# Optimization experiments

Measured on AMD Instinct MI355X. Metric: run time of the kernel, lower is better.

The kernel has to match this reference:

```python
import jax, jax.numpy as jnp
import numpy as np

N = 400000       # number of non-zero points
C_IN = 64
C_OUT = 64
K = 3            # kernel size per dim -> 27 offsets
S = 1024         # coordinate grid bound; packed key = ((x*S)+y)*S+z < 2^30 fits int32


def _pack(c):
    # linear packing: pack(a+b) == pack(a)+pack(b); injective for coords in [0, S-1]^3
    return (c[..., 0].astype(jnp.int32) * S + c[..., 1]) * S + c[..., 2]


def setup_inputs() -> dict:
    rng = np.random.default_rng(0)
    # unique coordinates in [1, S-2]^3 so coord+offset stays in [0, S-1]^3
    cand = rng.integers(1, S - 1, size=(2 * N, 3), dtype=np.int32)
    keys = (cand[:, 0].astype(np.int64) * S + cand[:, 1]) * S + cand[:, 2]
    _, uidx = np.unique(keys, return_index=True)
    coords = cand[np.sort(uidx)][:N]
    assert coords.shape[0] == N
    # kernel offsets: {-1,0,1}^3 in row-major (minuet layout order)
    r = np.arange(-(K // 2), K // 2 + 1)
    offsets = np.stack(np.meshgrid(r, r, r, indexing='ij'), axis=-1).reshape(-1, 3).astype(np.int32)
    key = jax.random.key(0)
    k1, k2 = jax.random.split(key)
    features = jax.random.normal(k1, (N, C_IN), dtype=jnp.float32)
    kernel = jax.random.normal(k2, (K ** 3, C_IN, C_OUT), dtype=jnp.float32) / np.float32(np.sqrt(C_IN * K ** 3))
    return {
        'features': features,
        'kernel': kernel,
        'coords': jnp.asarray(coords),
        'offsets': jnp.asarray(offsets),
    }


def reference(features, kernel, coords, offsets):
    # Sparse conv with stride=1: outputs live at the same (sorted) coordinates.
    # out_i = sum_k 1[p_j == q_i + delta_k] F_j @ W_k  (gather-GEMM-scatter)
    keys = _pack(coords)                      # [N]
    order = jnp.argsort(keys)                 # build sorted coordinate index
    skeys = keys[order]                       # [N] sorted keys
    sfeat = features[order]                   # [N, C_in]
    n = skeys.shape[0]
    okeys = _pack(offsets)                    # [K^3] packed offsets (linearity of _pack)

    def step(acc, xs):
        ok, Wk = xs                           # scalar key offset, [C_in, C_out]
        qk = skeys + ok                       # query keys = target coord + delta_k
        idx = jnp.clip(jnp.searchsorted(skeys, qk), 0, n - 1)
        valid = skeys[idx] == qk              # kernel-map mask for this offset
        g = jnp.where(valid[:, None], sfeat[idx], 0.0)   # gather
        return acc + g @ Wk, None             # GEMM + scatter(accumulate)

    out0 = jnp.zeros((n, kernel.shape[-1]), dtype=features.dtype)
    out, _ = jax.lax.scan(step, out0, (okeys, kernel))
    return out
```

## Files before the change

### kernel.cpp

```cpp
#include <hip/hip_runtime.h>

#define NBUCK  4096
#define SCAP   256
#define QCHUNK 256
#define WPAD   320
#define WCAP   (QCHUNK + 2 * WPAD + 16)
#define MCAP   96

typedef __bf16 bf16_t;
typedef bf16_t bf16x8 __attribute__((ext_vector_type(8)));
typedef float  f32x4  __attribute__((ext_vector_type(4)));
typedef unsigned long long u64;

__global__ void k_bin(const int* __restrict__ coords, const float* __restrict__ kern,
                      u64* __restrict__ slot, int* __restrict__ cnt,
                      bf16_t* __restrict__ wf, int N, int nb) {
    if (blockIdx.x >= nb) {
        int tid = (blockIdx.x - nb) * 256 + threadIdx.x;
        int f = tid >> 9, l = (tid >> 3) & 63, j = tid & 7;
        int nt = f >> 1, kt = f & 1;
        int k = kt * 32 + ((l >> 4) * 8) + j;
        int n = nt * 16 + (l & 15);
        wf[tid] = (bf16_t)kern[13 * 4096 + k * 64 + n];
        return;
    }
    __shared__ int sc[768];
    int base3 = blockIdx.x * 768;
    for (int t = threadIdx.x; t < 768; t += 256) {
        int idx = base3 + t;
        sc[t] = (idx < 3 * N) ? coords[idx] : 0;
    }
    __syncthreads();
    int i = blockIdx.x * 256 + threadIdx.x;
    if (i < N) {
        int key = (sc[3 * threadIdx.x] << 20) | (sc[3 * threadIdx.x + 1] << 10) | sc[3 * threadIdx.x + 2];
        int b = key >> 18;
        int pos = atomicAdd(&cnt[b], 1);
        if (pos < SCAP)
            slot[(size_t)b * SCAP + pos] = ((u64)(unsigned)key << 20) | (unsigned)i;
    }
}

__global__ void k_sortp(const int* __restrict__ cnt, const u64* __restrict__ slot,
                        int* __restrict__ skeys, int* __restrict__ sorder) {
    int t = threadIdx.x;
    int vals[16];
    int s = 0;
#pragma unroll
    for (int j = 0; j < 16; ++j) {
        int v = cnt[t * 16 + j];
        if (v > SCAP) v = SCAP;
        vals[j] = v; s += v;
    }
    int lane = t & 63, wv = t >> 6;
    int x = s;
#pragma unroll
    for (int d = 1; d < 64; d <<= 1) {
        int y = __shfl_up(x, d, 64);
        if (lane >= d) x += y;
    }
    __shared__ int wsum[4];
    if (lane == 63) wsum[wv] = x;
    __syncthreads();
    int add = 0;
    for (int u = 0; u < wv; ++u) add += wsum[u];
    int run = (x + add) - s;
    __shared__ int sbase[5];
    int b0 = blockIdx.x * 4;
#pragma unroll
    for (int j = 0; j < 16; ++j) {
        int bb = t * 16 + j;
        int d = bb - b0;
        if (d >= 0 && d <= 4) sbase[d] = run;
        run += vals[j];
    }
    if (t == 255 && b0 + 4 == NBUCK) sbase[4] = x + add;
    __syncthreads();

    __shared__ u64 sk[4][SCAP];
    int b = b0 + wv;
    int lo = sbase[wv];
    int size = sbase[wv + 1] - sbase[wv];
    for (int e = lane; e < size; e += 64) sk[wv][e] = slot[(size_t)b * SCAP + e];
    __syncthreads();
    for (int e = lane; e < size; e += 64) {
        u64 my = sk[wv][e];
        int r = 0;
        for (int j = 0; j < size; ++j) r += (sk[wv][j] < my);
        skeys[lo + r]  = (int)(my >> 20);
        sorder[lo + r] = (int)(my & 0xFFFFF);
    }
}

__device__ __forceinline__ int lower_bound_g(const int* __restrict__ a, int n, int q) {
    int lo = 0, hi = n;
    while (lo < hi) { int mid = (lo + hi) >> 1; if (a[mid] < q) lo = mid + 1; else hi = mid; }
    return lo;
}

__global__ __launch_bounds__(256) void k_conv(const int* __restrict__ skeys,
                                              const int* __restrict__ sorder,
                                              const float* __restrict__ feat,
                                              const bf16_t* __restrict__ wf,
                                              const float* __restrict__ kern,
                                              float* __restrict__ out, int N) {
    const int tid = threadIdx.x;
    const int lane = tid & 63, wv = tid >> 6;
    const int i0 = blockIdx.x * QCHUNK;
    const int iend = min(i0 + QCHUNK, N);

    __shared__ int sw[WCAP];
    __shared__ int mlist[MCAP * 3];
    __shared__ int mcount;
    if (tid == 0) mcount = 0;

    int i = i0 + tid;
    int kq = (i < iend) ? skeys[i] : 0;

    for (int w = 0; w < 3; ++w) {
        const int dx = w - 1;
        const int okdx = dx << 20;
        const long long drift = ((long long)okdx * N) >> 30;
        const int gw = (dx == 0) ? 16 : 96;
        int wlo = (int)max(0LL, (long long)i0 + drift - WPAD);
        int whi = (int)min((long long)N, (long long)iend + drift + WPAD);
        int wn = whi - wlo;
        __syncthreads();
        for (int t = tid; t < wn; t += 256) sw[t] = skeys[wlo + t];
        __syncthreads();
        int wfirst = sw[0], wlast = sw[wn - 1];

        if (i < iend) {
            int q0 = kq + okdx;
            int lok = q0 - 1025, hik = q0 + 1025;
            if (lok > wfirst && hik < wlast) {
                int p = (int)((long long)i + drift) - wlo;
                p = min(max(p, 0), wn - 1);
                int L = max(p - gw, 0), H = min(p + gw, wn - 1);
                if (!(sw[L] < lok && sw[H] >= lok)) { L = 0; H = wn - 1; }
                while (L < H) { int mid = (L + H) >> 1; if (sw[mid] < lok) L = mid + 1; else H = mid; }
                for (int pos = L; sw[pos] <= hik; ++pos) {
                    int d = sw[pos] - q0;
                    if (d == 0 && dx == 0) continue;
                    int dy, dz;
                    if (d >= -1 && d <= 1)             { dy = 0;  dz = d; }
                    else if (d >= 1023 && d <= 1025)   { dy = 1;  dz = d - 1024; }
                    else if (d >= -1025 && d <= -1023) { dy = -1; dz = d + 1024; }
                    else continue;
                    int kk = (dx + 1) * 9 + (dy + 1) * 3 + (dz + 1);
                    int tk = atomicAdd(&mcount, 1);
                    if (tk < MCAP) {
                        mlist[3 * tk] = i; mlist[3 * tk + 1] = sorder[wlo + pos]; mlist[3 * tk + 2] = kk;
                    }
                }
            } else {
                for (int dy = -1; dy <= 1; ++dy)
                    for (int dz = -1; dz <= 1; ++dz) {
                        if (dx == 0 && dy == 0 && dz == 0) continue;
                        int qt = q0 + dy * 1024 + dz;
                        int pos = lower_bound_g(skeys, N, qt);
                        if (pos < N && skeys[pos] == qt) {
                            int kk = (dx + 1) * 9 + (dy + 1) * 3 + (dz + 1);
                            int tk = atomicAdd(&mcount, 1);
                            if (tk < MCAP) {
                                mlist[3 * tk] = i; mlist[3 * tk + 1] = sorder[pos]; mlist[3 * tk + 2] = kk;
                            }
                        }
                    }
            }
        }
    }

    {
        const int m = lane & 15, quad = lane >> 4;
        for (int s = 0; s < QCHUNK / 64; ++s) {
            int tile = i0 + s * 64 + wv * 16;
            int srow = tile + m;
            int gi = (srow < N) ? srow : N - 1;
            int orig = sorder[gi];
            const float* rp = feat + (size_t)orig * 64;
            bf16x8 a[2];
#pragma unroll
            for (int kt = 0; kt < 2; ++kt) {
                const float* p = rp + kt * 32 + quad * 8;
                float4 x = *(const float4*)p;
                float4 y = *(const float4*)(p + 4);
                bf16x8 v;
                v[0] = (bf16_t)x.x; v[1] = (bf16_t)x.y; v[2] = (bf16_t)x.z; v[3] = (bf16_t)x.w;
                v[4] = (bf16_t)y.x; v[5] = (bf16_t)y.y; v[6] = (bf16_t)y.z; v[7] = (bf16_t)y.w;
                a[kt] = v;
            }
#pragma unroll
            for (int nt = 0; nt < 4; ++nt) {
                f32x4 acc = {0.f, 0.f, 0.f, 0.f};
#pragma unroll
                for (int kt = 0; kt < 2; ++kt) {
                    bf16x8 bfr = *(const bf16x8*)(wf + ((nt * 2 + kt) * 64 + lane) * 8);
                    acc = __builtin_amdgcn_mfma_f32_16x16x32_bf16(a[kt], bfr, acc, 0, 0, 0);
                }
#pragma unroll
                for (int r = 0; r < 4; ++r) {
                    int orow = tile + quad * 4 + r;
                    if (orow < iend) out[(size_t)orow * 64 + nt * 16 + m] = acc[r];
                }
            }
        }
    }
    __syncthreads();

    int ntask = min(mcount, MCAP);
    for (int t = wv; t < ntask; t += 4) {
        int dst = mlist[3 * t], src = mlist[3 * t + 1], wk = mlist[3 * t + 2];
        float f = feat[(size_t)src * 64 + lane];
        const float* W = kern + wk * 4096;
        float acc = 0.f;
#pragma unroll
        for (int cc = 0; cc < 64; ++cc)
            acc += __shfl(f, cc, 64) * W[cc * 64 + lane];
        atomicAdd(&out[(size_t)dst * 64 + lane], acc);
    }
}

extern "C" void kernel_launch(void* const* d_in, const int* in_sizes, int n_in,
                              void* d_out, int out_size, void* d_ws, size_t ws_size,
                              hipStream_t stream) {
    const float* feat   = (const float*)d_in[0];
    const float* kern   = (const float*)d_in[1];
    const int*   coords = (const int*)d_in[2];
    float* out = (float*)d_out;
    int N = in_sizes[0] / 64;

    char* w = (char*)d_ws;
    auto alloc = [&](size_t bytes) { char* p = w; w += (bytes + 255) & ~(size_t)255; return p; };
    u64* slot    = (u64*)alloc((size_t)NBUCK * SCAP * 8);
    int* skeys   = (int*)alloc((size_t)N * 4);
    int* sorder  = (int*)alloc((size_t)N * 4);
    int* cnt     = (int*)alloc(NBUCK * 4);
    bf16_t* wf   = (bf16_t*)alloc(4096 * 2);

    hipMemsetAsync(cnt, 0, NBUCK * 4, stream);

    int nb  = (N + 255) / 256;
    int nch = (N + QCHUNK - 1) / QCHUNK;
    k_bin  <<<nb + 16, 256, 0, stream>>>(coords, kern, slot, cnt, wf, N, nb);
    k_sortp<<<NBUCK / 4, 256, 0, stream>>>(cnt, slot, skeys, sorder);
    k_conv <<<nch, 256, 0, stream>>>(skeys, sorder, feat, wf, kern, out, N);
}
```

Measured before the change: 291.0 us.

## Stage all three window slices at once and software-pipeline feature loads

```diff
diff --git a/kernel.cpp b/kernel.cpp
--- a/kernel.cpp
+++ b/kernel.cpp
@@ -4,7 +4,7 @@
 #define SCAP   256
 #define QCHUNK 256
 #define WPAD   320
-#define WCAP   (QCHUNK + 2 * WPAD + 16)
+#define WSLOT  896
 #define MCAP   96
 
 typedef __bf16 bf16_t;
@@ -108,39 +108,62 @@
     const int lane = tid & 63, wv = tid >> 6;
     const int i0 = blockIdx.x * QCHUNK;
     const int iend = min(i0 + QCHUNK, N);
-
-    __shared__ int sw[WCAP];
+    const int m = lane & 15, quad = lane >> 4;
+
+    __shared__ int sw[3 * WSLOT];
     __shared__ int mlist[MCAP * 3];
     __shared__ int mcount;
     if (tid == 0) mcount = 0;
 
+    int origs[4];
+#pragma unroll
+    for (int s = 0; s < 4; ++s) {
+        int srow = i0 + s * 64 + wv * 16 + m;
+        origs[s] = sorder[(srow < N) ? srow : N - 1];
+    }
     int i = i0 + tid;
     int kq = (i < iend) ? skeys[i] : 0;
-
+    float4 c0, c1, c2, c3;
+    {
+        const float* rp = feat + (size_t)origs[0] * 64 + quad * 8;
+        c0 = *(const float4*)(rp);      c1 = *(const float4*)(rp + 4);
+        c2 = *(const float4*)(rp + 32); c3 = *(const float4*)(rp + 36);
+    }
+
+    int wloA[3], wnA[3];
+#pragma unroll
     for (int w = 0; w < 3; ++w) {
         const int dx = w - 1;
-        const int okdx = dx << 20;
-        const long long drift = ((long long)okdx * N) >> 30;
-        const int gw = (dx == 0) ? 16 : 96;
+        const long long drift = ((long long)(dx << 20) * N) >> 30;
         int wlo = (int)max(0LL, (long long)i0 + drift - WPAD);
         int whi = (int)min((long long)N, (long long)iend + drift + WPAD);
-        int wn = whi - wlo;
-        __syncthreads();
-        for (int t = tid; t < wn; t += 256) sw[t] = skeys[wlo + t];
-        __syncthreads();
-        int wfirst = sw[0], wlast = sw[wn - 1];
-
-        if (i < iend) {
+        wloA[w] = wlo; wnA[w] = whi - wlo;
+    }
+#pragma unroll
+    for (int w = 0; w < 3; ++w)
+        for (int t = tid; t < wnA[w]; t += 256) sw[w * WSLOT + t] = skeys[wloA[w] + t];
+    __syncthreads();
+
+    if (i < iend) {
+#pragma unroll
+        for (int w = 0; w < 3; ++w) {
+            const int dx = w - 1;
+            const int okdx = dx << 20;
+            const long long drift = ((long long)okdx * N) >> 30;
+            const int gw = (dx == 0) ? 16 : 96;
+            const int wlo = wloA[w], wn = wnA[w];
+            const int* swp = sw + w * WSLOT;
+            int wfirst = swp[0], wlast = swp[wn - 1];
             int q0 = kq + okdx;
             int lok = q0 - 1025, hik = q0 + 1025;
             if (lok > wfirst && hik < wlast) {
                 int p = (int)((long long)i + drift) - wlo;
                 p = min(max(p, 0), wn - 1);
                 int L = max(p - gw, 0), H = min(p + gw, wn - 1);
-                if (!(sw[L] < lok && sw[H] >= lok)) { L = 0; H = wn - 1; }
-                while (L < H) { int mid = (L + H) >> 1; if (sw[mid] < lok) L = mid + 1; else H = mid; }
-                for (int pos = L; sw[pos] <= hik; ++pos) {
-                    int d = sw[pos] - q0;
+                if (!(swp[L] < lok && swp[H] >= lok)) { L = 0; H = wn - 1; }
+                while (L < H) { int mid = (L + H) >> 1; if (swp[mid] < lok) L = mid + 1; else H = mid; }
+                for (int pos = L; swp[pos] <= hik; ++pos) {
+                    int d = swp[pos] - q0;
                     if (d == 0 && dx == 0) continue;
                     int dy, dz;
                     if (d >= -1 && d <= 1)             { dy = 0;  dz = d; }
@@ -171,40 +194,34 @@
         }
     }
 
-    {
-        const int m = lane & 15, quad = lane >> 4;
-        for (int s = 0; s < QCHUNK / 64; ++s) {
-            int tile = i0 + s * 64 + wv * 16;
-            int srow = tile + m;
-            int gi = (srow < N) ? srow : N - 1;
-            int orig = sorder[gi];
-            const float* rp = feat + (size_t)orig * 64;
-            bf16x8 a[2];
-#pragma unroll
-            for (int kt = 0; kt < 2; ++kt) {
-                const float* p = rp + kt * 32 + quad * 8;
-                float4 x = *(const float4*)p;
-                float4 y = *(const float4*)(p + 4);
-                bf16x8 v;
-                v[0] = (bf16_t)x.x; v[1] = (bf16_t)x.y; v[2] = (bf16_t)x.z; v[3] = (bf16_t)x.w;
-                v[4] = (bf16_t)y.x; v[5] = (bf16_t)y.y; v[6] = (bf16_t)y.z; v[7] = (bf16_t)y.w;
-                a[kt] = v;
-            }
-#pragma unroll
-            for (int nt = 0; nt < 4; ++nt) {
-                f32x4 acc = {0.f, 0.f, 0.f, 0.f};
-#pragma unroll
-                for (int kt = 0; kt < 2; ++kt) {
-                    bf16x8 bfr = *(const bf16x8*)(wf + ((nt * 2 + kt) * 64 + lane) * 8);
-                    acc = __builtin_amdgcn_mfma_f32_16x16x32_bf16(a[kt], bfr, acc, 0, 0, 0);
-                }
-#pragma unroll
-                for (int r = 0; r < 4; ++r) {
-                    int orow = tile + quad * 4 + r;
-                    if (orow < iend) out[(size_t)orow * 64 + nt * 16 + m] = acc[r];
-                }
+#pragma unroll
+    for (int s = 0; s < 4; ++s) {
+        float4 n0, n1, n2, n3;
+        if (s < 3) {
+            const float* rp = feat + (size_t)origs[s + 1] * 64 + quad * 8;
+            n0 = *(const float4*)(rp);      n1 = *(const float4*)(rp + 4);
+            n2 = *(const float4*)(rp + 32); n3 = *(const float4*)(rp + 36);
+        }
+        bf16x8 a0, a1;
+        a0[0] = (bf16_t)c0.x; a0[1] = (bf16_t)c0.y; a0[2] = (bf16_t)c0.z; a0[3] = (bf16_t)c0.w;
+        a0[4] = (bf16_t)c1.x; a0[5] = (bf16_t)c1.y; a0[6] = (bf16_t)c1.z; a0[7] = (bf16_t)c1.w;
+        a1[0] = (bf16_t)c2.x; a1[1] = (bf16_t)c2.y; a1[2] = (bf16_t)c2.z; a1[3] = (bf16_t)c2.w;
+        a1[4] = (bf16_t)c3.x; a1[5] = (bf16_t)c3.y; a1[6] = (bf16_t)c3.z; a1[7] = (bf16_t)c3.w;
+        int tile = i0 + s * 64 + wv * 16;
+#pragma unroll
+        for (int nt = 0; nt < 4; ++nt) {
+            f32x4 acc = {0.f, 0.f, 0.f, 0.f};
+            bf16x8 b0 = *(const bf16x8*)(wf + ((nt * 2 + 0) * 64 + lane) * 8);
+            bf16x8 b1 = *(const bf16x8*)(wf + ((nt * 2 + 1) * 64 + lane) * 8);
+            acc = __builtin_amdgcn_mfma_f32_16x16x32_bf16(a0, b0, acc, 0, 0, 0);
+            acc = __builtin_amdgcn_mfma_f32_16x16x32_bf16(a1, b1, acc, 0, 0, 0);
+#pragma unroll
+            for (int r = 0; r < 4; ++r) {
+                int orow = tile + quad * 4 + r;
+                if (orow < iend) out[(size_t)orow * 64 + nt * 16 + m] = acc[r];
             }
         }
+        if (s < 3) { c0 = n0; c1 = n1; c2 = n2; c3 = n3; }
     }
     __syncthreads();
 
```

After: 288.1 us. Within noise of the previous version (-1.0%).
